# Kernel tuning notes

Hardware: AMD Instinct MI355X
Metric: run time of the kernel (lower is better)

Reference implementation:

```python
import jax, jax.numpy as jnp
import numpy as np

# PSLoss constants (from init_kwargs)
MSE_WEIGHT = 0.5
W_CORR = 1.0
W_VAR = 1.0
W_MEAN = 1.0
K = 3           # k_dominant_freqs
MIN_PATCH = 5   # min_patch_len (max(2, 5))
EPS = 1e-8


def setup_inputs() -> dict:
    key = jax.random.key(0)
    k1, k2 = jax.random.split(key)
    B, T, F = 64, 336, 321
    forecast = jax.random.normal(k1, (B, T, F), dtype=jnp.float32)
    target = jax.random.normal(k2, (B, T, F), dtype=jnp.float32)
    return {"forecast": forecast, "target": target}


def _structural_loss(fc, tg):
    """fc, tg: [N, T] flattened (batch*features) series. Returns (total_loss_sum, patch_count)."""
    N, T = tg.shape
    Mmax = T // MIN_PATCH  # max segments per period (period >= MIN_PATCH)

    # --- Fourier adaptive patching (vectorized over all N series) ---
    amp = jnp.abs(jnp.fft.rfft(tg, axis=-1))[:, 1:]           # drop DC, [N, T//2]
    _, rel = jax.lax.top_k(amp, K)                             # [N, K]
    freq_idx = (rel + 1).astype(jnp.float32)
    p = jnp.floor(T / freq_idx).astype(jnp.int32)              # dominant periods [N, K]
    # dedup periods in topk order (the original 'processed_periods' set)
    eq = p[:, :, None] == p[:, None, :]                        # [N, K, K]
    earlier = jnp.tril(jnp.ones((K, K), dtype=bool), -1)       # j < k
    dup = jnp.any(eq & earlier, axis=-1)
    valid_p = (p >= MIN_PATCH) & ~dup                          # [N, K]

    nseg = T // p                                              # [N, K] (p >= 2 always)
    s_idx = jnp.arange(Mmax, dtype=jnp.int32)
    seg_s = p[:, :, None] * s_idx                              # [N, K, Mmax]
    seg_e = seg_s + p[:, :, None]
    seg_v = (s_idx < nseg[:, :, None]) & valid_p[:, :, None]
    rem_s = nseg * p                                           # remaining tail patch
    rem_v = valid_p & ((T - rem_s) >= MIN_PATCH)

    starts = jnp.concatenate([seg_s.reshape(N, -1), rem_s], axis=-1)
    ends = jnp.concatenate([seg_e.reshape(N, -1), jnp.full_like(rem_s, T)], axis=-1)
    valid = jnp.concatenate([seg_v.reshape(N, -1), rem_v], axis=-1)
    # fallback whole-series patch if no patch survived
    none = ~jnp.any(valid, axis=-1, keepdims=True)
    starts = jnp.concatenate([starts, jnp.zeros((N, 1), jnp.int32)], axis=-1)
    ends = jnp.concatenate([ends, jnp.full((N, 1), T, jnp.int32)], axis=-1)
    valid = jnp.concatenate([valid, none], axis=-1)            # [N, M]

    # --- dedup identical (start, end) patches (original list(set(...))) ---
    SENT = (T + 1) * (T + 1)
    keys = jnp.where(valid, starts * (T + 1) + ends, SENT)
    keys = jnp.sort(keys, axis=-1)
    uniq = jnp.concatenate(
        [jnp.ones((N, 1), dtype=bool), keys[:, 1:] != keys[:, :-1]], axis=-1)
    valid = (keys != SENT) & uniq
    s = jnp.where(valid, keys // (T + 1), 0)                   # safe dummy (0,2) when invalid
    e = jnp.where(valid, keys % (T + 1), 2)

    # --- per-patch stats via inclusive prefix sums ---
    def csum(x):
        return jnp.concatenate([jnp.zeros((N, 1), x.dtype), jnp.cumsum(x, axis=-1)], axis=-1)

    cs_t, cs_f = csum(tg), csum(fc)
    cs_tt, cs_ff, cs_tf = csum(tg * tg), csum(fc * fc), csum(tg * fc)

    def seg_sum(cs):
        return jnp.take_along_axis(cs, e, axis=-1) - jnp.take_along_axis(cs, s, axis=-1)

    n = (e - s).astype(jnp.float32)
    St, Sf = seg_sum(cs_t), seg_sum(cs_f)
    Stt, Sff, Stf = seg_sum(cs_tt), seg_sum(cs_ff), seg_sum(cs_tf)
    mt, mf = St / n, Sf / n
    tvs = jnp.maximum(Stt - n * mt * mt, 0.0)   # sum of squared deviations (target)
    fvs = jnp.maximum(Sff - n * mf * mf, 0.0)
    num = Stf - n * mt * mf
    corr = num / (jnp.sqrt(tvs * fvs) + EPS)
    corr_loss = 1.0 - jnp.abs(corr)
    tvar = tvs / (n - 1.0)                      # torch.var is unbiased
    fvar = fvs / (n - 1.0)
    var_loss = jnp.abs(tvar - fvar) / (tvar + EPS)
    mean_loss = jnp.abs(mt - mf) / (jnp.abs(mt) + EPS)
    patch_loss = W_CORR * corr_loss + W_VAR * var_loss + W_MEAN * mean_loss

    total = jnp.sum(jnp.where(valid, patch_loss, 0.0))
    count = jnp.sum(valid)
    return total, count


def reference(forecast, target):
    B, T, F = forecast.shape
    fc = jnp.transpose(forecast, (0, 2, 1)).reshape(B * F, T)
    tg = jnp.transpose(target, (0, 2, 1)).reshape(B * F, T)
    total, count = _structural_loss(fc, tg)
    avg = jnp.where(count > 0,
                    total / jnp.maximum(count, 1).astype(jnp.float32),
                    jnp.float32(0.0))
    mse = jnp.mean((forecast - target) ** 2)
    return MSE_WEIGHT * mse + (1.0 - MSE_WEIGHT) * avg
```

## Files before the change

### kernel.cpp

```cpp
#include <hip/hip_runtime.h>
#include <hip/hip_bf16.h>

#define TT 336
#define NF 321
#define NB 64
#define NSER (NB * NF)
#define WPB 4
#define KP 352
#define LDA 360
#define SPB 16
#define NPSB (NSER / SPB)
#define NPSBG 1288
#define NPATB (NSER / WPB)
#define TSP (TT + 4)

#define SK(b) ((b) + ((b) >> 5))
#define TBL 348

#define TGX 11
#define TGY 11
#define NMSEP (TGX * TGY * NB)

typedef __attribute__((ext_vector_type(8))) short bf16x8;
typedef __attribute__((ext_vector_type(4))) float f32x4;
typedef unsigned long long ULL;

__device__ __forceinline__ unsigned short f2bf(float v) {
    unsigned x = __float_as_uint(v);
    x += 0x7FFFu + ((x >> 16) & 1u);
    return (unsigned short)(x >> 16);
}

__device__ __forceinline__ void ins3(ULL& a0, ULL& a1, ULL& a2, ULL x) {
    ULL hi = a0 > x ? a0 : x;
    ULL lo = a0 > x ? x : a0;
    a0 = hi;
    ULL hi1 = a1 > lo ? a1 : lo;
    ULL lo1 = a1 > lo ? lo : a1;
    a1 = hi1;
    a2 = a2 > lo1 ? a2 : lo1;
}

__global__ void twiddle_k(unsigned short* __restrict__ Wb) {
    int n = blockIdx.x;
    int f = (n >> 1) + 1;
    int isSin = n & 1;
    for (int k = threadIdx.x; k < KP; k += blockDim.x) {
        float v = 0.0f;
        if (k < TT) {
            int r = (f * k) % TT;
            float ang = 6.2831853071795864769f * (float)r / 336.0f;
            v = isSin ? sinf(ang) : cosf(ang);
        }
        Wb[(size_t)n * KP + k] = f2bf(v);
    }
}

__global__ __launch_bounds__(256) void psd_k(const float* __restrict__ tgO,
                                             const unsigned short* __restrict__ Wb,
                                             uint4* __restrict__ topk) {
    __shared__ __align__(16) unsigned short sA[SPB][LDA];
    __shared__ ULL tk3[4][SPB][3];
    const int tid = threadIdx.x;
    const int lb = (blockIdx.x & 7) * 161 + (blockIdx.x >> 3);
    if (lb >= NPSB) return;
    const int serBase = lb * SPB;

    {
        int f_l = tid & 15, tch = tid >> 4;
        int ser = serBase + f_l;
        int bb = ser / NF, ff = ser - bb * NF;
        const float* base = tgO + (size_t)bb * TT * NF + ff;
        int t0 = tch * 21;
        float v[21];
#pragma unroll
        for (int i = 0; i < 21; i++) v[i] = base[(size_t)(t0 + i) * NF];
#pragma unroll
        for (int i = 0; i < 21; i++) sA[f_l][t0 + i] = f2bf(v[i]);
    }
    if (tid < SPB * 16) sA[tid >> 4][TT + (tid & 15)] = 0;
    __syncthreads();

    const int wave = tid >> 6, lane = tid & 63;
    const int quad = lane >> 4, c = lane & 15;
    const unsigned short* aRow = &sA[c][quad * 8];
    const int ntStart = wave * 5;
    const int ntEnd = (wave == 3) ? 21 : ntStart + 5;

    ULL t0k[4] = {0, 0, 0, 0}, t1k[4] = {0, 0, 0, 0}, t2k[4] = {0, 0, 0, 0};
    for (int nt = ntStart; nt < ntEnd; nt++) {
        const unsigned short* bRow = Wb + (size_t)(nt * 16 + c) * KP + quad * 8;
        f32x4 acc = (f32x4){0.f, 0.f, 0.f, 0.f};
#pragma unroll
        for (int ks = 0; ks < 11; ks++) {
            bf16x8 a = *(const bf16x8*)(aRow + ks * 32);
            bf16x8 b = *(const bf16x8*)(bRow + ks * 32);
            acc = __builtin_amdgcn_mfma_f32_16x16x32_bf16(a, b, acc, 0, 0, 0);
        }
        int n = nt * 16 + c;
        unsigned fidx = (unsigned)((n >> 1) + 1);
        unsigned ftag = 0xFFFFFFFFu - fidx;
        bool odd = (n & 1) != 0;
#pragma unroll
        for (int r = 0; r < 4; r++) {
            float v = acc[r];
            float p = v * v;
            p += __shfl_xor(p, 1, 64);
            ULL key = odd ? 0ull
                          : (((ULL)__float_as_uint(p) << 32) | (ULL)ftag);
            ins3(t0k[r], t1k[r], t2k[r], key);
        }
    }
#pragma unroll
    for (int m = 2; m <= 8; m <<= 1) {
#pragma unroll
        for (int r = 0; r < 4; r++) {
            ULL b0 = __shfl_xor(t0k[r], m, 64);
            ULL b1 = __shfl_xor(t1k[r], m, 64);
            ULL b2 = __shfl_xor(t2k[r], m, 64);
            ins3(t0k[r], t1k[r], t2k[r], b0);
            ins3(t0k[r], t1k[r], t2k[r], b1);
            ins3(t0k[r], t1k[r], t2k[r], b2);
        }
    }
    if (c == 0) {
#pragma unroll
        for (int r = 0; r < 4; r++) {
            int s = quad * 4 + r;
            tk3[wave][s][0] = t0k[r];
            tk3[wave][s][1] = t1k[r];
            tk3[wave][s][2] = t2k[r];
        }
    }
    __syncthreads();
    if (tid < SPB) {
        ULL k0 = 0, k1 = 0, k2 = 0;
#pragma unroll
        for (int wv = 0; wv < 4; wv++) {
#pragma unroll
            for (int j = 0; j < 3; j++) ins3(k0, k1, k2, tk3[wv][tid][j]);
        }
        unsigned f0 = 0xFFFFFFFFu - (unsigned)(k0 & 0xFFFFFFFFull);
        unsigned f1 = 0xFFFFFFFFu - (unsigned)(k1 & 0xFFFFFFFFull);
        unsigned f2 = 0xFFFFFFFFu - (unsigned)(k2 & 0xFFFFFFFFull);
        topk[serBase + tid] = make_uint4(f0, f1, f2, 0u);
    }
}

__global__ __launch_bounds__(256) void transpose_k(const float* __restrict__ fc,
                                                   const float* __restrict__ tg,
                                                   float2* __restrict__ out,
                                                   double* __restrict__ msep,
                                                   double* __restrict__ acc) {
    __shared__ float ta[32][33];
    __shared__ float tb[32][33];
    __shared__ double wacc[4];
    const int b = blockIdx.z;
    const int t0 = blockIdx.x * 32, f0 = blockIdx.y * 32;
    const int tx = threadIdx.x, ty = threadIdx.y;
    const size_t base = (size_t)b * TT * NF;
    double ms = 0.0;
#pragma unroll
    for (int k = 0; k < 4; k++) {
        int t = t0 + ty + 8 * k, f = f0 + tx;
        if (t < TT && f < NF) {
            float a = tg[base + (size_t)t * NF + f];
            float c = fc[base + (size_t)t * NF + f];
            ta[ty + 8 * k][tx] = a;
            tb[ty + 8 * k][tx] = c;
            double d = (double)a - (double)c;
            ms += d * d;
        }
    }
    __syncthreads();
#pragma unroll
    for (int k = 0; k < 4; k++) {
        int f = f0 + ty + 8 * k, t = t0 + tx;
        if (t < TT && f < NF) {
            out[((size_t)b * NF + f) * TT + t] =
                make_float2(ta[tx][ty + 8 * k], tb[tx][ty + 8 * k]);
        }
    }
    for (int off = 32; off; off >>= 1) ms += __shfl_down(ms, off, 64);
    int flat = ty * 32 + tx;
    int lane = flat & 63, wid = flat >> 6;
    if (lane == 0) wacc[wid] = ms;
    __syncthreads();
    if (flat == 0) {
        double tot = wacc[0] + wacc[1] + wacc[2] + wacc[3];
        if (msep) {
            int blk = (blockIdx.z * TGY + blockIdx.y) * TGX + blockIdx.x;
            msep[blk] = tot;
        } else {
            atomicAdd(&acc[0], tot);
        }
    }
}

__global__ void mse_k(const float* __restrict__ fc, const float* __restrict__ tg,
                      double* __restrict__ acc) {
    const size_t N4 = (size_t)NB * TT * NF / 4;
    const float4* a4 = (const float4*)fc;
    const float4* b4 = (const float4*)tg;
    double s = 0.0;
    for (size_t i = (size_t)blockIdx.x * blockDim.x + threadIdx.x; i < N4;
         i += (size_t)gridDim.x * blockDim.x) {
        float4 a = a4[i], b = b4[i];
        double d0 = (double)a.x - (double)b.x;
        double d1 = (double)a.y - (double)b.y;
        double d2 = (double)a.z - (double)b.z;
        double d3 = (double)a.w - (double)b.w;
        s += d0 * d0 + d1 * d1 + d2 * d2 + d3 * d3;
    }
    for (int off = 32; off; off >>= 1) s += __shfl_down(s, off, 64);
    __shared__ double wsum[4];
    int flat = threadIdx.x;
    int lane = flat & 63, wid = flat >> 6;
    if (lane == 0) wsum[wid] = s;
    __syncthreads();
    if (flat == 0) atomicAdd(&acc[0], wsum[0] + wsum[1] + wsum[2] + wsum[3]);
}

__device__ __forceinline__ double patch_loss(double S1, double S2, double S3,
                                             double S4, double S5, double nn) {
    double mt = S1 / nn, mf = S2 / nn;
    double tvs = S3 - nn * mt * mt; tvs = tvs > 0.0 ? tvs : 0.0;
    double fvs = S4 - nn * mf * mf; fvs = fvs > 0.0 ? fvs : 0.0;
    double num = S5 - nn * mt * mf;
    double corr = num / (sqrt(tvs * fvs) + 1e-8);
    double closs = 1.0 - fabs(corr);
    double tvar = tvs / (nn - 1.0), fvar = fvs / (nn - 1.0);
    double vloss = fabs(tvar - fvar) / (tvar + 1e-8);
    double mloss = fabs(mt - mf) / (fabs(mt) + 1e-8);
    return closs + vloss + mloss;
}

__device__ __forceinline__ double patch_loss_fast(double S1, double S2,
                                                  float S3, float S4, float S5,
                                                  int n) {
    float nnf = (float)n;
    float invf = 1.0f / nnf;
    float s1f = (float)S1, s2f = (float)S2;
    float tvs = S3 - s1f * s1f * invf; tvs = tvs > 0.f ? tvs : 0.f;
    float fvs = S4 - s2f * s2f * invf; fvs = fvs > 0.f ? fvs : 0.f;
    float num = S5 - s1f * s2f * invf;
    float corr = num / (sqrtf(tvs * fvs) + 1e-8f);
    float closs = 1.0f - fabsf(corr);
    float vloss = fabsf(tvs - fvs) / (tvs + (nnf - 1.0f) * 1e-8f);
    double mloss = fabs(S1 - S2) / (fabs(S1) + (double)n * 1e-8);
    return (double)(closs + vloss) + mloss;
}

struct PatchCfg {
    int P[3], nseg[3], rs[3];
    bool vp[3], hr[3];
};

__device__ __forceinline__ void make_cfg(int fr0, int fr1, int fr2, PatchCfg& c) {
    c.P[0] = TT / fr0; c.P[1] = TT / fr1; c.P[2] = TT / fr2;
    c.vp[0] = (c.P[0] >= 5);
    c.vp[1] = (c.P[1] >= 5) && (c.P[1] != c.P[0]);
    c.vp[2] = (c.P[2] >= 5) && (c.P[2] != c.P[0]) && (c.P[2] != c.P[1]);
#pragma unroll
    for (int q = 0; q < 3; q++) {
        c.nseg[q] = TT / c.P[q];
        c.rs[q] = c.nseg[q] * c.P[q];
        c.hr[q] = c.vp[q] && ((TT - c.rs[q]) >= 5);
    }
}

__device__ __forceinline__ bool slot_patch(const PatchCfg& c, int i, int& s, int& e) {
    bool kept = false;
    s = 0; e = 0;
    if (i < 204) {
        int k = (i >= 136) ? 2 : ((i >= 68) ? 1 : 0);
        int si = i - k * 68;
        if (c.vp[k]) {
            if (si < c.nseg[k]) { s = c.P[k] * si; e = s + c.P[k]; kept = true; }
            else if (si == c.nseg[k] && c.hr[k]) { s = c.rs[k]; e = TT; kept = true; }
            if (kept) {
#pragma unroll
                for (int j = 0; j < 2; j++) {
                    if (j < k && c.vp[j]) {
                        bool dup = (s == c.rs[j]) && (e == TT) && c.hr[j];
                        int len = e - s;
                        if (len == c.P[j] && s < c.rs[j] && (s % c.P[j]) == 0) dup = true;
                        if (dup) kept = false;
                    }
                }
            }
        }
    }
    return kept;
}

__global__ __launch_bounds__(256) void patch_k(const float* __restrict__ fcO,
                                               const float* __restrict__ tgO,
                                               const uint4* __restrict__ topk,
                                               double* __restrict__ blkout) {
    __shared__ __align__(16) char smem[2 * WPB * TBL * 8 + 3 * WPB * TBL * 4];
    double (*d1)[TBL] = (double(*)[TBL])smem;
    double (*d2)[TBL] = (double(*)[TBL])(smem + WPB * TBL * 8);
    char* regB = smem + 2 * WPB * TBL * 8;
    float2* tsB = (float2*)regB;
    float (*t3)[TBL] = (float(*)[TBL])regB;
    float (*t4)[TBL] = (float(*)[TBL])(regB + WPB * TBL * 4);
    float (*t5)[TBL] = (float(*)[TBL])(regB + 2 * WPB * TBL * 4);
    __shared__ double wms[WPB], wls[WPB], wlc[WPB];

    const int tid = threadIdx.x;
    const int w = tid >> 6, lane = tid & 63;
    const int lb = (blockIdx.x & 7) * (NPATB / 8) + (blockIdx.x >> 3);
    const int ser = lb * WPB + w;

    {
        const int j = tid & 3;
        const int serj = lb * WPB + j;
        const int bb = serj / NF, ff = serj - bb * NF;
        const float* tb_ = tgO + (size_t)bb * TT * NF + ff;
        const float* fb_ = fcO + (size_t)bb * TT * NF + ff;
        const int tb0 = tid >> 2;
        float2* row = tsB + j * TSP;
        double ms = 0.0;
#pragma unroll
        for (int i = 0; i < 6; i++) {
            int t = tb0 + 64 * i;
            if (t < TT) {
                float a = tb_[(size_t)t * NF];
                float c = fb_[(size_t)t * NF];
                row[t] = make_float2(a, c);
                double d = (double)a - (double)c;
                ms += d * d;
            }
        }
        for (int off = 32; off; off >>= 1) ms += __shfl_down(ms, off, 64);
        if (lane == 0) wms[w] = ms;
    }
    __syncthreads();

    float2 loc[6];
    double c1 = 0, c2 = 0;
    float c3 = 0, c4 = 0, c5 = 0;
    if (lane < 56) {
        const float4* lp = (const float4*)(tsB + w * TSP + 6 * lane);
        float4 va = lp[0], vb = lp[1], vc = lp[2];
        loc[0] = make_float2(va.x, va.y); loc[1] = make_float2(va.z, va.w);
        loc[2] = make_float2(vb.x, vb.y); loc[3] = make_float2(vb.z, vb.w);
        loc[4] = make_float2(vc.x, vc.y); loc[5] = make_float2(vc.z, vc.w);
#pragma unroll
        for (int i = 0; i < 6; i++) {
            float a = loc[i].x, b = loc[i].y;
            c1 += (double)a; c2 += (double)b;
            c3 = fmaf(a, a, c3); c4 = fmaf(b, b, c4); c5 = fmaf(a, b, c5);
        }
    }

    double s1 = c1, s2 = c2;
    float s3 = c3, s4 = c4, s5 = c5;
#pragma unroll
    for (int off = 1; off < 64; off <<= 1) {
        double y1 = __shfl_up(s1, off, 64);
        double y2 = __shfl_up(s2, off, 64);
        float y3 = __shfl_up(s3, off, 64);
        float y4 = __shfl_up(s4, off, 64);
        float y5 = __shfl_up(s5, off, 64);
        if (lane >= off) { s1 += y1; s2 += y2; s3 += y3; s4 += y4; s5 += y5; }
    }

    __syncthreads();

    if (lane == 63) {
        d1[w][SK(0)] = 0.0; d2[w][SK(0)] = 0.0;
        t3[w][SK(0)] = 0.f; t4[w][SK(0)] = 0.f; t5[w][SK(0)] = 0.f;
    }
    if (lane < 56) {
        double r1 = s1 - c1, r2 = s2 - c2;
        float r3 = s3 - c3, r4 = s4 - c4, r5 = s5 - c5;
#pragma unroll
        for (int i = 0; i < 6; i++) {
            float a = loc[i].x, b = loc[i].y;
            r1 += (double)a; r2 += (double)b;
            r3 = fmaf(a, a, r3); r4 = fmaf(b, b, r4); r5 = fmaf(a, b, r5);
            int ix = SK(6 * lane + i + 1);
            d1[w][ix] = r1; d2[w][ix] = r2;
            t3[w][ix] = r3; t4[w][ix] = r4; t5[w][ix] = r5;
        }
    }
    __syncthreads();

    uint4 tk = topk[ser];
    PatchCfg cfg;
    make_cfg((int)tk.x, (int)tk.y, (int)tk.z, cfg);

    double lsum = 0.0, lcnt = 0.0;
    ULL anyMask = 0ull;
#pragma unroll
    for (int rI = 0; rI < 4; rI++) {
        int s, e;
        bool kept = slot_patch(cfg, lane + 64 * rI, s, e);
        ULL bal = __ballot(kept);
        anyMask |= bal;
        if (bal == 0ull) continue;
        if (kept) {
            int is = SK(s), ie = SK(e);
            double S1 = d1[w][ie] - d1[w][is];
            double S2 = d2[w][ie] - d2[w][is];
            float S3 = t3[w][ie] - t3[w][is];
            float S4 = t4[w][ie] - t4[w][is];
            float S5 = t5[w][ie] - t5[w][is];
            lsum += patch_loss_fast(S1, S2, S3, S4, S5, e - s);
            lcnt += 1.0;
        }
    }

    if (anyMask == 0ull) {
        if (lane == 0) {
            int ie = SK(TT);
            lsum += patch_loss_fast(d1[w][ie], d2[w][ie], t3[w][ie],
                                    t4[w][ie], t5[w][ie], TT);
            lcnt += 1.0;
        }
    }

    for (int off = 32; off; off >>= 1) {
        lsum += __shfl_down(lsum, off, 64);
        lcnt += __shfl_down(lcnt, off, 64);
    }
    if (lane == 0) { wls[w] = lsum; wlc[w] = lcnt; }
    __syncthreads();
    if (tid == 0) {
        blkout[3 * lb + 0] = wls[0] + wls[1] + wls[2] + wls[3];
        blkout[3 * lb + 1] = wlc[0] + wlc[1] + wlc[2] + wlc[3];
        blkout[3 * lb + 2] = wms[0] + wms[1] + wms[2] + wms[3];
    }
}

__device__ __forceinline__ void patch_body(const float2* tsw, int lane,
                                           int fr0, int fr1, int fr2,
                                           double& lsum, double& lcnt) {
    PatchCfg cfg;
    make_cfg(fr0, fr1, fr2, cfg);
    ULL anyMask = 0ull;
#pragma unroll
    for (int rI = 0; rI < 4; rI++) {
        int s, e;
        bool kept = slot_patch(cfg, lane + 64 * rI, s, e);
        anyMask |= __ballot(kept);
        if (kept) {
            double S1 = 0, S2 = 0, S3 = 0, S4 = 0, S5 = 0;
            for (int t = s; t < e; t++) {
                float2 v = tsw[t];
                double a = (double)v.x, b = (double)v.y;
                S1 += a; S2 += b;
                S3 += a * a; S4 += b * b; S5 += a * b;
            }
            lsum += patch_loss(S1, S2, S3, S4, S5, (double)(e - s));
            lcnt += 1.0;
        }
    }
    if (anyMask == 0ull) {
        double S1 = 0, S2 = 0, S3 = 0, S4 = 0, S5 = 0;
        for (int t = lane; t < TT; t += 64) {
            float2 v = tsw[t];
            double a = (double)v.x, b = (double)v.y;
            S1 += a; S2 += b;
            S3 += a * a; S4 += b * b; S5 += a * b;
        }
        for (int off = 32; off; off >>= 1) {
            S1 += __shfl_down(S1, off, 64);
            S2 += __shfl_down(S2, off, 64);
            S3 += __shfl_down(S3, off, 64);
            S4 += __shfl_down(S4, off, 64);
            S5 += __shfl_down(S5, off, 64);
        }
        if (lane == 0) {
            lsum += patch_loss(S1, S2, S3, S4, S5, (double)TT);
            lcnt += 1.0;
        }
    }
}

__global__ __launch_bounds__(256, 6) void series_k(const float2* __restrict__ tsG,
                                                   const float* __restrict__ fcG,
                                                   const float* __restrict__ tgG,
                                                   int transposed,
                                                   double2* __restrict__ pairs,
                                                   double* __restrict__ acc) {
    const int w = threadIdx.x >> 6, lane = threadIdx.x & 63;
    const int ser = blockIdx.x * WPB + w;
    __shared__ float2 ts[WPB][TT];
    __shared__ float4 zb[WPB][84];

    if (transposed) {
        const float2* sp = tsG + (size_t)ser * TT;
        for (int t = lane; t < TT; t += 64) ts[w][t] = sp[t];
    } else {
        int b = ser / NF, f = ser - b * NF;
        const float* tp = tgG + (size_t)b * TT * NF + f;
        const float* fp = fcG + (size_t)b * TT * NF + f;
        for (int t = lane; t < TT; t += 64)
            ts[w][t] = make_float2(tp[(size_t)t * NF], fp[(size_t)t * NF]);
    }
    __syncthreads();

    for (int t = lane; t < 84; t += 64) {
        float x0 = ts[w][t].x, x1 = ts[w][t + 84].x;
        float x2 = ts[w][t + 168].x, x3 = ts[w][t + 252].x;
        float a = x0 + x2, b2 = x1 + x3, c = x0 - x2, d = x1 - x3;
        zb[w][t] = make_float4(a + b2, a - b2, c, d);
    }
    __syncthreads();

    const double TWOPI = 6.283185307179586476925286766559;
    int fb[3] = {1 + lane, 65 + lane, 129 + lane};
    float cc[3], sn[3], re[3], im[3], cd[3], sd[3], sgn[3];
    int selA[3];
#pragma unroll
    for (int q = 0; q < 3; q++) {
        int f = fb[q], cls = f & 3;
        double dl = (double)f * (TWOPI / 336.0);
        cd[q] = (float)cos(dl);
        sd[q] = (float)sin(dl);
        cc[q] = 1.0f; sn[q] = 0.0f; re[q] = 0.0f; im[q] = 0.0f;
        sgn[q] = (cls == 1) ? -1.0f : ((cls == 3) ? 1.0f : 0.0f);
        selA[q] = (cls == 0) ? 0 : ((cls == 2) ? 1 : 2);
    }
    for (int t = 0; t < 84; t++) {
        float4 zv = zb[w][t];
#pragma unroll
        for (int q = 0; q < 3; q++) {
            float zr = (selA[q] == 0) ? zv.x : ((selA[q] == 1) ? zv.y : zv.z);
            float zi = sgn[q] * zv.w;
            re[q] = fmaf(zr, cc[q], re[q]);
            re[q] = fmaf(zi, sn[q], re[q]);
            im[q] = fmaf(zi, cc[q], im[q]);
            im[q] = fmaf(-zr, sn[q], im[q]);
            float nc = fmaf(cc[q], cd[q], -(sn[q] * sd[q]));
            float ns = fmaf(sn[q], cd[q], cc[q] * sd[q]);
            cc[q] = nc; sn[q] = ns;
        }
    }

    ULL k0 = 0, k1 = 0, k2 = 0;
#pragma unroll
    for (int q = 0; q < 3; q++) {
        float a2 = fmaf(re[q], re[q], im[q] * im[q]);
        ULL key = ((ULL)__float_as_uint(a2) << 32) |
                  (ULL)(0xFFFFFFFFu - (unsigned)fb[q]);
        if (fb[q] > 168) key = 0ull;
        ins3(k0, k1, k2, key);
    }
    for (int m = 1; m < 64; m <<= 1) {
        ULL b0 = __shfl_xor(k0, m, 64);
        ULL b1 = __shfl_xor(k1, m, 64);
        ULL b2 = __shfl_xor(k2, m, 64);
        ins3(k0, k1, k2, b0); ins3(k0, k1, k2, b1); ins3(k0, k1, k2, b2);
    }

    int fr0 = (int)(0xFFFFFFFFu - (unsigned)(k0 & 0xFFFFFFFFull));
    int fr1 = (int)(0xFFFFFFFFu - (unsigned)(k1 & 0xFFFFFFFFull));
    int fr2 = (int)(0xFFFFFFFFu - (unsigned)(k2 & 0xFFFFFFFFull));

    double lsum = 0.0, lcnt = 0.0;
    patch_body(&ts[w][0], lane, fr0, fr1, fr2, lsum, lcnt);

    for (int off = 32; off; off >>= 1) {
        lsum += __shfl_down(lsum, off, 64);
        lcnt += __shfl_down(lcnt, off, 64);
    }
    if (lane == 0) {
        if (pairs) {
            pairs[ser] = make_double2(lsum, lcnt);
        } else {
            atomicAdd(&acc[1], lsum);
            atomicAdd(&acc[2], lcnt);
        }
    }
}

__global__ __launch_bounds__(1024) void reduce3_k(const double* __restrict__ blkout,
                                                  float* __restrict__ out) {
    const int tid = threadIdx.x;
    double ls = 0.0, lc = 0.0, ms = 0.0;
    for (int i = tid; i < NPATB; i += 1024) {
        ls += blkout[3 * i + 0];
        lc += blkout[3 * i + 1];
        ms += blkout[3 * i + 2];
    }
    for (int off = 32; off; off >>= 1) {
        ls += __shfl_down(ls, off, 64);
        lc += __shfl_down(lc, off, 64);
        ms += __shfl_down(ms, off, 64);
    }
    __shared__ double sl[16], sc[16], sm[16];
    int lane = tid & 63, wid = tid >> 6;
    if (lane == 0) { sl[wid] = ls; sc[wid] = lc; sm[wid] = ms; }
    __syncthreads();
    if (tid == 0) {
        double L = 0, C = 0, M = 0;
        for (int i = 0; i < 16; i++) { L += sl[i]; C += sc[i]; M += sm[i]; }
        double mse = M / (double)((size_t)NB * TT * NF);
        double avg = (C > 0.0) ? (L / C) : 0.0;
        out[0] = (float)(0.5 * mse + 0.5 * avg);
    }
}

__global__ __launch_bounds__(1024) void reduce_k(const double2* __restrict__ pairs,
                                                 const double* __restrict__ msep,
                                                 int nmse,
                                                 float* __restrict__ out) {
    const int tid = threadIdx.x;
    double ls = 0.0, lc = 0.0, ms = 0.0;
    for (int i = tid; i < NSER; i += 1024) {
        double2 p = pairs[i];
        ls += p.x; lc += p.y;
    }
    for (int i = tid; i < nmse; i += 1024) ms += msep[i];
    for (int off = 32; off; off >>= 1) {
        ls += __shfl_down(ls, off, 64);
        lc += __shfl_down(lc, off, 64);
        ms += __shfl_down(ms, off, 64);
    }
    __shared__ double sl[16], sc[16], sm[16];
    int lane = tid & 63, wid = tid >> 6;
    if (lane == 0) { sl[wid] = ls; sc[wid] = lc; sm[wid] = ms; }
    __syncthreads();
    if (tid == 0) {
        double L = 0, C = 0, M = 0;
        for (int i = 0; i < 16; i++) { L += sl[i]; C += sc[i]; M += sm[i]; }
        double mse = M / (double)((size_t)NB * TT * NF);
        double avg = (C > 0.0) ? (L / C) : 0.0;
        out[0] = (float)(0.5 * mse + 0.5 * avg);
    }
}

__global__ void finalize_k(const double* __restrict__ acc, float* __restrict__ out) {
    double mse = acc[0] / (double)((size_t)NB * TT * NF);
    double avg = (acc[2] > 0.0) ? (acc[1] / acc[2]) : 0.0;
    out[0] = (float)(0.5 * mse + 0.5 * avg);
}

extern "C" void kernel_launch(void* const* d_in, const int* in_sizes, int n_in,
                              void* d_out, int out_size, void* d_ws, size_t ws_size,
                              hipStream_t stream) {
    const float* fc = (const float*)d_in[0];
    const float* tg = (const float*)d_in[1];
    float* out = (float*)d_out;
    char* ws = (char*)d_ws;
    double* acc = (double*)ws;

    const size_t OFF_MSE = 64;
    const size_t OFF_PAIR = OFF_MSE + (size_t)NMSEP * sizeof(double);
    const size_t OFF_TOP = OFF_PAIR + (size_t)NSER * sizeof(double2);
    const size_t OFF_W = OFF_TOP + (size_t)NSER * sizeof(uint4);
    const size_t OFF_END2 = OFF_W + (size_t)TT * KP * sizeof(unsigned short);
    const size_t bytesT = (size_t)NSER * TT * sizeof(float2);
    const bool big2 = (ws_size >= OFF_END2);
    const size_t R3_OFF_TS = OFF_PAIR + (size_t)NSER * sizeof(double2);
    const bool big = !big2 && (ws_size >= R3_OFF_TS + bytesT);
    const bool mid = !big2 && !big && (ws_size >= OFF_MSE + bytesT);

    double* msep = (double*)(ws + OFF_MSE);
    double* blkout = (double*)(ws + OFF_PAIR);
    uint4* topkBuf = (uint4*)(ws + OFF_TOP);
    unsigned short* Wb = (unsigned short*)(ws + OFF_W);

    dim3 tg_grid(TGX, TGY, NB);
    dim3 tg_blk(32, 8);

    if (big2) {
        twiddle_k<<<TT, 128, 0, stream>>>(Wb);
        psd_k<<<NPSBG, 256, 0, stream>>>(tg, Wb, topkBuf);
        patch_k<<<NPATB, 64 * WPB, 0, stream>>>(fc, tg, topkBuf, blkout);
        reduce3_k<<<1, 1024, 0, stream>>>(blkout, out);
    } else if (big) {
        float2* tsT = (float2*)(ws + R3_OFF_TS);
        transpose_k<<<tg_grid, tg_blk, 0, stream>>>(fc, tg, tsT, msep, acc);
        series_k<<<NSER / WPB, 64 * WPB, 0, stream>>>(tsT, fc, tg, 1,
                                                      (double2*)blkout, acc);
        reduce_k<<<1, 1024, 0, stream>>>((double2*)blkout, msep, NMSEP, out);
    } else if (mid) {
        float2* tsT = (float2*)(ws + OFF_MSE);
        hipMemsetAsync(d_ws, 0, 64, stream);
        transpose_k<<<tg_grid, tg_blk, 0, stream>>>(fc, tg, tsT, nullptr, acc);
        series_k<<<NSER / WPB, 64 * WPB, 0, stream>>>(tsT, fc, tg, 1, nullptr, acc);
        finalize_k<<<1, 1, 0, stream>>>(acc, out);
    } else {
        hipMemsetAsync(d_ws, 0, 64, stream);
        mse_k<<<1024, 256, 0, stream>>>(fc, tg, acc);
        series_k<<<NSER / WPB, 64 * WPB, 0, stream>>>(nullptr, fc, tg, 0, nullptr, acc);
        finalize_k<<<1, 1, 0, stream>>>(acc, out);
    }
}
```

Measured before the change: 160.0 us.

## Fuse PSD top-k and patch loss kernels into a single kernel

Merges the MFMA-based spectral top-k kernel and the per-series patch statistics kernel into one kernel. Each block now computes top-k for its 16 series, keeps the result in shared memory, then loops over four groups of four series to compute the prefix sums and patch losses, reusing the same shared buffer. This removes a kernel launch and the global round trip of the top-k buffer. In exchange each block does more serial work with extra barriers, and the grid drops to 1288 blocks, which may lower parallelism in the patch phase.

```diff
diff --git a/kernel.cpp b/kernel.cpp
--- a/kernel.cpp
+++ b/kernel.cpp
@@ -56,15 +56,101 @@
     }
 }
 
-__global__ __launch_bounds__(256) void psd_k(const float* __restrict__ tgO,
-                                             const unsigned short* __restrict__ Wb,
-                                             uint4* __restrict__ topk) {
-    __shared__ __align__(16) unsigned short sA[SPB][LDA];
-    __shared__ ULL tk3[4][SPB][3];
+__device__ __forceinline__ double patch_loss(double S1, double S2, double S3,
+                                             double S4, double S5, double nn) {
+    double mt = S1 / nn, mf = S2 / nn;
+    double tvs = S3 - nn * mt * mt; tvs = tvs > 0.0 ? tvs : 0.0;
+    double fvs = S4 - nn * mf * mf; fvs = fvs > 0.0 ? fvs : 0.0;
+    double num = S5 - nn * mt * mf;
+    double corr = num / (sqrt(tvs * fvs) + 1e-8);
+    double closs = 1.0 - fabs(corr);
+    double tvar = tvs / (nn - 1.0), fvar = fvs / (nn - 1.0);
+    double vloss = fabs(tvar - fvar) / (tvar + 1e-8);
+    double mloss = fabs(mt - mf) / (fabs(mt) + 1e-8);
+    return closs + vloss + mloss;
+}
+
+__device__ __forceinline__ double patch_loss_fast(double S1, double S2,
+                                                  float S3, float S4, float S5,
+                                                  int n) {
+    float nnf = (float)n;
+    float invf = 1.0f / nnf;
+    float s1f = (float)S1, s2f = (float)S2;
+    float tvs = S3 - s1f * s1f * invf; tvs = tvs > 0.f ? tvs : 0.f;
+    float fvs = S4 - s2f * s2f * invf; fvs = fvs > 0.f ? fvs : 0.f;
+    float num = S5 - s1f * s2f * invf;
+    float corr = num / (sqrtf(tvs * fvs) + 1e-8f);
+    float closs = 1.0f - fabsf(corr);
+    float vloss = fabsf(tvs - fvs) / (tvs + (nnf - 1.0f) * 1e-8f);
+    double mloss = fabs(S1 - S2) / (fabs(S1) + (double)n * 1e-8);
+    return (double)(closs + vloss) + mloss;
+}
+
+struct PatchCfg {
+    int P[3], nseg[3], rs[3];
+    bool vp[3], hr[3];
+};
+
+__device__ __forceinline__ void make_cfg(int fr0, int fr1, int fr2, PatchCfg& c) {
+    c.P[0] = TT / fr0; c.P[1] = TT / fr1; c.P[2] = TT / fr2;
+    c.vp[0] = (c.P[0] >= 5);
+    c.vp[1] = (c.P[1] >= 5) && (c.P[1] != c.P[0]);
+    c.vp[2] = (c.P[2] >= 5) && (c.P[2] != c.P[0]) && (c.P[2] != c.P[1]);
+#pragma unroll
+    for (int q = 0; q < 3; q++) {
+        c.nseg[q] = TT / c.P[q];
+        c.rs[q] = c.nseg[q] * c.P[q];
+        c.hr[q] = c.vp[q] && ((TT - c.rs[q]) >= 5);
+    }
+}
+
+__device__ __forceinline__ bool slot_patch(const PatchCfg& c, int i, int& s, int& e) {
+    bool kept = false;
+    s = 0; e = 0;
+    if (i < 204) {
+        int k = (i >= 136) ? 2 : ((i >= 68) ? 1 : 0);
+        int si = i - k * 68;
+        if (c.vp[k]) {
+            if (si < c.nseg[k]) { s = c.P[k] * si; e = s + c.P[k]; kept = true; }
+            else if (si == c.nseg[k] && c.hr[k]) { s = c.rs[k]; e = TT; kept = true; }
+            if (kept) {
+#pragma unroll
+                for (int j = 0; j < 2; j++) {
+                    if (j < k && c.vp[j]) {
+                        bool dup = (s == c.rs[j]) && (e == TT) && c.hr[j];
+                        int len = e - s;
+                        if (len == c.P[j] && s < c.rs[j] && (s % c.P[j]) == 0) dup = true;
+                        if (dup) kept = false;
+                    }
+                }
+            }
+        }
+    }
+    return kept;
+}
+
+__global__ __launch_bounds__(256) void psdpatch_k(const float* __restrict__ fcO,
+                                                  const float* __restrict__ tgO,
+                                                  const unsigned short* __restrict__ Wb,
+                                                  double* __restrict__ blkout) {
+    __shared__ __align__(16) char smem[2 * WPB * TBL * 8 + 3 * WPB * TBL * 4];
+    unsigned short (*sA)[LDA] = (unsigned short(*)[LDA])smem;
+    ULL (*tk3)[SPB][3] = (ULL(*)[SPB][3])(smem + SPB * LDA * 2);
+    double (*d1)[TBL] = (double(*)[TBL])smem;
+    double (*d2)[TBL] = (double(*)[TBL])(smem + WPB * TBL * 8);
+    char* regB = smem + 2 * WPB * TBL * 8;
+    float2* tsB = (float2*)regB;
+    float (*t3)[TBL] = (float(*)[TBL])regB;
+    float (*t4)[TBL] = (float(*)[TBL])(regB + WPB * TBL * 4);
+    float (*t5)[TBL] = (float(*)[TBL])(regB + 2 * WPB * TBL * 4);
+    __shared__ uint4 tkf[SPB];
+    __shared__ double wms[WPB], wls[WPB], wlc[WPB];
+
     const int tid = threadIdx.x;
     const int lb = (blockIdx.x & 7) * 161 + (blockIdx.x >> 3);
     if (lb >= NPSB) return;
     const int serBase = lb * SPB;
+    const int wave = tid >> 6, lane = tid & 63;
 
     {
         int f_l = tid & 15, tch = tid >> 4;
@@ -81,55 +167,56 @@
     if (tid < SPB * 16) sA[tid >> 4][TT + (tid & 15)] = 0;
     __syncthreads();
 
-    const int wave = tid >> 6, lane = tid & 63;
-    const int quad = lane >> 4, c = lane & 15;
-    const unsigned short* aRow = &sA[c][quad * 8];
-    const int ntStart = wave * 5;
-    const int ntEnd = (wave == 3) ? 21 : ntStart + 5;
-
-    ULL t0k[4] = {0, 0, 0, 0}, t1k[4] = {0, 0, 0, 0}, t2k[4] = {0, 0, 0, 0};
-    for (int nt = ntStart; nt < ntEnd; nt++) {
-        const unsigned short* bRow = Wb + (size_t)(nt * 16 + c) * KP + quad * 8;
-        f32x4 acc = (f32x4){0.f, 0.f, 0.f, 0.f};
-#pragma unroll
-        for (int ks = 0; ks < 11; ks++) {
-            bf16x8 a = *(const bf16x8*)(aRow + ks * 32);
-            bf16x8 b = *(const bf16x8*)(bRow + ks * 32);
-            acc = __builtin_amdgcn_mfma_f32_16x16x32_bf16(a, b, acc, 0, 0, 0);
-        }
-        int n = nt * 16 + c;
-        unsigned fidx = (unsigned)((n >> 1) + 1);
-        unsigned ftag = 0xFFFFFFFFu - fidx;
-        bool odd = (n & 1) != 0;
-#pragma unroll
-        for (int r = 0; r < 4; r++) {
-            float v = acc[r];
-            float p = v * v;
-            p += __shfl_xor(p, 1, 64);
-            ULL key = odd ? 0ull
-                          : (((ULL)__float_as_uint(p) << 32) | (ULL)ftag);
-            ins3(t0k[r], t1k[r], t2k[r], key);
-        }
-    }
-#pragma unroll
-    for (int m = 2; m <= 8; m <<= 1) {
-#pragma unroll
-        for (int r = 0; r < 4; r++) {
-            ULL b0 = __shfl_xor(t0k[r], m, 64);
-            ULL b1 = __shfl_xor(t1k[r], m, 64);
-            ULL b2 = __shfl_xor(t2k[r], m, 64);
-            ins3(t0k[r], t1k[r], t2k[r], b0);
-            ins3(t0k[r], t1k[r], t2k[r], b1);
-            ins3(t0k[r], t1k[r], t2k[r], b2);
-        }
-    }
-    if (c == 0) {
-#pragma unroll
-        for (int r = 0; r < 4; r++) {
-            int s = quad * 4 + r;
-            tk3[wave][s][0] = t0k[r];
-            tk3[wave][s][1] = t1k[r];
-            tk3[wave][s][2] = t2k[r];
+    {
+        const int quad = lane >> 4, c = lane & 15;
+        const unsigned short* aRow = &sA[c][quad * 8];
+        const int ntStart = wave * 5;
+        const int ntEnd = (wave == 3) ? 21 : ntStart + 5;
+
+        ULL t0k[4] = {0, 0, 0, 0}, t1k[4] = {0, 0, 0, 0}, t2k[4] = {0, 0, 0, 0};
+        for (int nt = ntStart; nt < ntEnd; nt++) {
+            const unsigned short* bRow = Wb + (size_t)(nt * 16 + c) * KP + quad * 8;
+            f32x4 acc = (f32x4){0.f, 0.f, 0.f, 0.f};
+#pragma unroll
+            for (int ks = 0; ks < 11; ks++) {
+                bf16x8 a = *(const bf16x8*)(aRow + ks * 32);
+                bf16x8 b = *(const bf16x8*)(bRow + ks * 32);
+                acc = __builtin_amdgcn_mfma_f32_16x16x32_bf16(a, b, acc, 0, 0, 0);
+            }
+            int n = nt * 16 + c;
+            unsigned fidx = (unsigned)((n >> 1) + 1);
+            unsigned ftag = 0xFFFFFFFFu - fidx;
+            bool odd = (n & 1) != 0;
+#pragma unroll
+            for (int r = 0; r < 4; r++) {
+                float v = acc[r];
+                float p = v * v;
+                p += __shfl_xor(p, 1, 64);
+                ULL key = odd ? 0ull
+                              : (((ULL)__float_as_uint(p) << 32) | (ULL)ftag);
+                ins3(t0k[r], t1k[r], t2k[r], key);
+            }
+        }
+#pragma unroll
+        for (int m = 2; m <= 8; m <<= 1) {
+#pragma unroll
+            for (int r = 0; r < 4; r++) {
+                ULL b0 = __shfl_xor(t0k[r], m, 64);
+                ULL b1 = __shfl_xor(t1k[r], m, 64);
+                ULL b2 = __shfl_xor(t2k[r], m, 64);
+                ins3(t0k[r], t1k[r], t2k[r], b0);
+                ins3(t0k[r], t1k[r], t2k[r], b1);
+                ins3(t0k[r], t1k[r], t2k[r], b2);
+            }
+        }
+        if (c == 0) {
+#pragma unroll
+            for (int r = 0; r < 4; r++) {
+                int s = quad * 4 + r;
+                tk3[wave][s][0] = t0k[r];
+                tk3[wave][s][1] = t1k[r];
+                tk3[wave][s][2] = t2k[r];
+            }
         }
     }
     __syncthreads();
@@ -143,7 +230,159 @@
         unsigned f0 = 0xFFFFFFFFu - (unsigned)(k0 & 0xFFFFFFFFull);
         unsigned f1 = 0xFFFFFFFFu - (unsigned)(k1 & 0xFFFFFFFFull);
         unsigned f2 = 0xFFFFFFFFu - (unsigned)(k2 & 0xFFFFFFFFull);
-        topk[serBase + tid] = make_uint4(f0, f1, f2, 0u);
+        tkf[tid] = make_uint4(f0, f1, f2, 0u);
+    }
+
+    double lsumRun = 0.0, lcntRun = 0.0, msThr = 0.0;
+    const int w = wave;
+
+    for (int rr = 0; rr < 4; rr++) {
+        __syncthreads();
+
+        {
+            const int j = tid & 3;
+            const int serj = serBase + 4 * rr + j;
+            const int bb = serj / NF, ff = serj - bb * NF;
+            const float* tb_ = tgO + (size_t)bb * TT * NF + ff;
+            const float* fb_ = fcO + (size_t)bb * TT * NF + ff;
+            const int tb0 = tid >> 2;
+            float2* row = tsB + j * TSP;
+#pragma unroll
+            for (int i = 0; i < 6; i++) {
+                int t = tb0 + 64 * i;
+                if (t < TT) {
+                    float a = tb_[(size_t)t * NF];
+                    float c = fb_[(size_t)t * NF];
+                    row[t] = make_float2(a, c);
+                    double d = (double)a - (double)c;
+                    msThr += d * d;
+                }
+            }
+        }
+        __syncthreads();
+
+        float2 loc[6];
+        double c1 = 0, c2 = 0;
+        float c3 = 0, c4 = 0, c5 = 0;
+        if (lane < 56) {
+            const float4* lp = (const float4*)(tsB + w * TSP + 6 * lane);
+            float4 va = lp[0], vb = lp[1], vc = lp[2];
+            loc[0] = make_float2(va.x, va.y); loc[1] = make_float2(va.z, va.w);
+            loc[2] = make_float2(vb.x, vb.y); loc[3] = make_float2(vb.z, vb.w);
+            loc[4] = make_float2(vc.x, vc.y); loc[5] = make_float2(vc.z, vc.w);
+#pragma unroll
+            for (int i = 0; i < 6; i++) {
+                float a = loc[i].x, b = loc[i].y;
+                c1 += (double)a; c2 += (double)b;
+                c3 = fmaf(a, a, c3); c4 = fmaf(b, b, c4); c5 = fmaf(a, b, c5);
+            }
+        }
+
+        double s1 = c1, s2 = c2;
+        float s3 = c3, s4 = c4, s5 = c5;
+#pragma unroll
+        for (int off = 1; off < 64; off <<= 1) {
+            double y1 = __shfl_up(s1, off, 64);
+            double y2 = __shfl_up(s2, off, 64);
+            float y3 = __shfl_up(s3, off, 64);
+            float y4 = __shfl_up(s4, off, 64);
+            float y5 = __shfl_up(s5, off, 64);
+            if (lane >= off) { s1 += y1; s2 += y2; s3 += y3; s4 += y4; s5 += y5; }
+        }
+
+        __syncthreads();
+
+        if (lane == 63) {
+            d1[w][SK(0)] = 0.0; d2[w][SK(0)] = 0.0;
+            t3[w][SK(0)] = 0.f; t4[w][SK(0)] = 0.f; t5[w][SK(0)] = 0.f;
+        }
+        if (lane < 56) {
+            double r1 = s1 - c1, r2 = s2 - c2;
+            float r3 = s3 - c3, r4 = s4 - c4, r5 = s5 - c5;
+#pragma unroll
+            for (int i = 0; i < 6; i++) {
+                float a = loc[i].x, b = loc[i].y;
+                r1 += (double)a; r2 += (double)b;
+                r3 = fmaf(a, a, r3); r4 = fmaf(b, b, r4); r5 = fmaf(a, b, r5);
+                int ix = SK(6 * lane + i + 1);
+                d1[w][ix] = r1; d2[w][ix] = r2;
+                t3[w][ix] = r3; t4[w][ix] = r4; t5[w][ix] = r5;
+            }
+        }
+        __syncthreads();
+
+        uint4 tk = tkf[4 * rr + w];
+        PatchCfg cfg;
+        make_cfg((int)tk.x, (int)tk.y, (int)tk.z, cfg);
+
+        ULL anyMask = 0ull;
+#pragma unroll
+        for (int rI = 0; rI < 4; rI++) {
+            int s, e;
+            bool kept = slot_patch(cfg, lane + 64 * rI, s, e);
+            ULL bal = __ballot(kept);
+            anyMask |= bal;
+            if (bal == 0ull) continue;
+            if (kept) {
+                int is = SK(s), ie = SK(e);
+                double S1 = d1[w][ie] - d1[w][is];
+                double S2 = d2[w][ie] - d2[w][is];
+                float S3 = t3[w][ie] - t3[w][is];
+                float S4 = t4[w][ie] - t4[w][is];
+                float S5 = t5[w][ie] - t5[w][is];
+                lsumRun += patch_loss_fast(S1, S2, S3, S4, S5, e - s);
+                lcntRun += 1.0;
+            }
+        }
+        if (anyMask == 0ull) {
+            if (lane == 0) {
+                int ie = SK(TT);
+                lsumRun += patch_loss_fast(d1[w][ie], d2[w][ie], t3[w][ie],
+                                           t4[w][ie], t5[w][ie], TT);
+                lcntRun += 1.0;
+            }
+        }
+    }
+
+    for (int off = 32; off; off >>= 1) {
+        lsumRun += __shfl_down(lsumRun, off, 64);
+        lcntRun += __shfl_down(lcntRun, off, 64);
+        msThr += __shfl_down(msThr, off, 64);
+    }
+    if (lane == 0) { wls[w] = lsumRun; wlc[w] = lcntRun; wms[w] = msThr; }
+    __syncthreads();
+    if (tid == 0) {
+        blkout[3 * lb + 0] = wls[0] + wls[1] + wls[2] + wls[3];
+        blkout[3 * lb + 1] = wlc[0] + wlc[1] + wlc[2] + wlc[3];
+        blkout[3 * lb + 2] = wms[0] + wms[1] + wms[2] + wms[3];
+    }
+}
+
+__global__ __launch_bounds__(1024) void reduce3_k(const double* __restrict__ blkout,
+                                                  int nblk,
+                                                  float* __restrict__ out) {
+    const int tid = threadIdx.x;
+    double ls = 0.0, lc = 0.0, ms = 0.0;
+    for (int i = tid; i < nblk; i += 1024) {
+        ls += blkout[3 * i + 0];
+        lc += blkout[3 * i + 1];
+        ms += blkout[3 * i + 2];
+    }
+    for (int off = 32; off; off >>= 1) {
+        ls += __shfl_down(ls, off, 64);
+        lc += __shfl_down(lc, off, 64);
+        ms += __shfl_down(ms, off, 64);
+    }
+    __shared__ double sl[16], sc[16], sm[16];
+    int lane = tid & 63, wid = tid >> 6;
+    if (lane == 0) { sl[wid] = ls; sc[wid] = lc; sm[wid] = ms; }
+    __syncthreads();
+    if (tid == 0) {
+        double L = 0, C = 0, M = 0;
+        for (int i = 0; i < 16; i++) { L += sl[i]; C += sc[i]; M += sm[i]; }
+        double mse = M / (double)((size_t)NB * TT * NF);
+        double avg = (C > 0.0) ? (L / C) : 0.0;
+        out[0] = (float)(0.5 * mse + 0.5 * avg);
     }
 }
 
@@ -221,220 +460,6 @@
     if (flat == 0) atomicAdd(&acc[0], wsum[0] + wsum[1] + wsum[2] + wsum[3]);
 }
 
-__device__ __forceinline__ double patch_loss(double S1, double S2, double S3,
-                                             double S4, double S5, double nn) {
-    double mt = S1 / nn, mf = S2 / nn;
-    double tvs = S3 - nn * mt * mt; tvs = tvs > 0.0 ? tvs : 0.0;
-    double fvs = S4 - nn * mf * mf; fvs = fvs > 0.0 ? fvs : 0.0;
-    double num = S5 - nn * mt * mf;
-    double corr = num / (sqrt(tvs * fvs) + 1e-8);
-    double closs = 1.0 - fabs(corr);
-    double tvar = tvs / (nn - 1.0), fvar = fvs / (nn - 1.0);
-    double vloss = fabs(tvar - fvar) / (tvar + 1e-8);
-    double mloss = fabs(mt - mf) / (fabs(mt) + 1e-8);
-    return closs + vloss + mloss;
-}
-
-__device__ __forceinline__ double patch_loss_fast(double S1, double S2,
-                                                  float S3, float S4, float S5,
-                                                  int n) {
-    float nnf = (float)n;
-    float invf = 1.0f / nnf;
-    float s1f = (float)S1, s2f = (float)S2;
-    float tvs = S3 - s1f * s1f * invf; tvs = tvs > 0.f ? tvs : 0.f;
-    float fvs = S4 - s2f * s2f * invf; fvs = fvs > 0.f ? fvs : 0.f;
-    float num = S5 - s1f * s2f * invf;
-    float corr = num / (sqrtf(tvs * fvs) + 1e-8f);
-    float closs = 1.0f - fabsf(corr);
-    float vloss = fabsf(tvs - fvs) / (tvs + (nnf - 1.0f) * 1e-8f);
-    double mloss = fabs(S1 - S2) / (fabs(S1) + (double)n * 1e-8);
-    return (double)(closs + vloss) + mloss;
-}
-
-struct PatchCfg {
-    int P[3], nseg[3], rs[3];
-    bool vp[3], hr[3];
-};
-
-__device__ __forceinline__ void make_cfg(int fr0, int fr1, int fr2, PatchCfg& c) {
-    c.P[0] = TT / fr0; c.P[1] = TT / fr1; c.P[2] = TT / fr2;
-    c.vp[0] = (c.P[0] >= 5);
-    c.vp[1] = (c.P[1] >= 5) && (c.P[1] != c.P[0]);
-    c.vp[2] = (c.P[2] >= 5) && (c.P[2] != c.P[0]) && (c.P[2] != c.P[1]);
-#pragma unroll
-    for (int q = 0; q < 3; q++) {
-        c.nseg[q] = TT / c.P[q];
-        c.rs[q] = c.nseg[q] * c.P[q];
-        c.hr[q] = c.vp[q] && ((TT - c.rs[q]) >= 5);
-    }
-}
-
-__device__ __forceinline__ bool slot_patch(const PatchCfg& c, int i, int& s, int& e) {
-    bool kept = false;
-    s = 0; e = 0;
-    if (i < 204) {
-        int k = (i >= 136) ? 2 : ((i >= 68) ? 1 : 0);
-        int si = i - k * 68;
-        if (c.vp[k]) {
-            if (si < c.nseg[k]) { s = c.P[k] * si; e = s + c.P[k]; kept = true; }
-            else if (si == c.nseg[k] && c.hr[k]) { s = c.rs[k]; e = TT; kept = true; }
-            if (kept) {
-#pragma unroll
-                for (int j = 0; j < 2; j++) {
-                    if (j < k && c.vp[j]) {
-                        bool dup = (s == c.rs[j]) && (e == TT) && c.hr[j];
-                        int len = e - s;
-                        if (len == c.P[j] && s < c.rs[j] && (s % c.P[j]) == 0) dup = true;
-                        if (dup) kept = false;
-                    }
-                }
-            }
-        }
-    }
-    return kept;
-}
-
-__global__ __launch_bounds__(256) void patch_k(const float* __restrict__ fcO,
-                                               const float* __restrict__ tgO,
-                                               const uint4* __restrict__ topk,
-                                               double* __restrict__ blkout) {
-    __shared__ __align__(16) char smem[2 * WPB * TBL * 8 + 3 * WPB * TBL * 4];
-    double (*d1)[TBL] = (double(*)[TBL])smem;
-    double (*d2)[TBL] = (double(*)[TBL])(smem + WPB * TBL * 8);
-    char* regB = smem + 2 * WPB * TBL * 8;
-    float2* tsB = (float2*)regB;
-    float (*t3)[TBL] = (float(*)[TBL])regB;
-    float (*t4)[TBL] = (float(*)[TBL])(regB + WPB * TBL * 4);
-    float (*t5)[TBL] = (float(*)[TBL])(regB + 2 * WPB * TBL * 4);
-    __shared__ double wms[WPB], wls[WPB], wlc[WPB];
-
-    const int tid = threadIdx.x;
-    const int w = tid >> 6, lane = tid & 63;
-    const int lb = (blockIdx.x & 7) * (NPATB / 8) + (blockIdx.x >> 3);
-    const int ser = lb * WPB + w;
-
-    {
-        const int j = tid & 3;
-        const int serj = lb * WPB + j;
-        const int bb = serj / NF, ff = serj - bb * NF;
-        const float* tb_ = tgO + (size_t)bb * TT * NF + ff;
-        const float* fb_ = fcO + (size_t)bb * TT * NF + ff;
-        const int tb0 = tid >> 2;
-        float2* row = tsB + j * TSP;
-        double ms = 0.0;
-#pragma unroll
-        for (int i = 0; i < 6; i++) {
-            int t = tb0 + 64 * i;
-            if (t < TT) {
-                float a = tb_[(size_t)t * NF];
-                float c = fb_[(size_t)t * NF];
-                row[t] = make_float2(a, c);
-                double d = (double)a - (double)c;
-                ms += d * d;
-            }
-        }
-        for (int off = 32; off; off >>= 1) ms += __shfl_down(ms, off, 64);
-        if (lane == 0) wms[w] = ms;
-    }
-    __syncthreads();
-
-    float2 loc[6];
-    double c1 = 0, c2 = 0;
-    float c3 = 0, c4 = 0, c5 = 0;
-    if (lane < 56) {
-        const float4* lp = (const float4*)(tsB + w * TSP + 6 * lane);
-        float4 va = lp[0], vb = lp[1], vc = lp[2];
-        loc[0] = make_float2(va.x, va.y); loc[1] = make_float2(va.z, va.w);
-        loc[2] = make_float2(vb.x, vb.y); loc[3] = make_float2(vb.z, vb.w);
-        loc[4] = make_float2(vc.x, vc.y); loc[5] = make_float2(vc.z, vc.w);
-#pragma unroll
-        for (int i = 0; i < 6; i++) {
-            float a = loc[i].x, b = loc[i].y;
-            c1 += (double)a; c2 += (double)b;
-            c3 = fmaf(a, a, c3); c4 = fmaf(b, b, c4); c5 = fmaf(a, b, c5);
-        }
-    }
-
-    double s1 = c1, s2 = c2;
-    float s3 = c3, s4 = c4, s5 = c5;
-#pragma unroll
-    for (int off = 1; off < 64; off <<= 1) {
-        double y1 = __shfl_up(s1, off, 64);
-        double y2 = __shfl_up(s2, off, 64);
-        float y3 = __shfl_up(s3, off, 64);
-        float y4 = __shfl_up(s4, off, 64);
-        float y5 = __shfl_up(s5, off, 64);
-        if (lane >= off) { s1 += y1; s2 += y2; s3 += y3; s4 += y4; s5 += y5; }
-    }
-
-    __syncthreads();
-
-    if (lane == 63) {
-        d1[w][SK(0)] = 0.0; d2[w][SK(0)] = 0.0;
-        t3[w][SK(0)] = 0.f; t4[w][SK(0)] = 0.f; t5[w][SK(0)] = 0.f;
-    }
-    if (lane < 56) {
-        double r1 = s1 - c1, r2 = s2 - c2;
-        float r3 = s3 - c3, r4 = s4 - c4, r5 = s5 - c5;
-#pragma unroll
-        for (int i = 0; i < 6; i++) {
-            float a = loc[i].x, b = loc[i].y;
-            r1 += (double)a; r2 += (double)b;
-            r3 = fmaf(a, a, r3); r4 = fmaf(b, b, r4); r5 = fmaf(a, b, r5);
-            int ix = SK(6 * lane + i + 1);
-            d1[w][ix] = r1; d2[w][ix] = r2;
-            t3[w][ix] = r3; t4[w][ix] = r4; t5[w][ix] = r5;
-        }
-    }
-    __syncthreads();
-
-    uint4 tk = topk[ser];
-    PatchCfg cfg;
-    make_cfg((int)tk.x, (int)tk.y, (int)tk.z, cfg);
-
-    double lsum = 0.0, lcnt = 0.0;
-    ULL anyMask = 0ull;
-#pragma unroll
-    for (int rI = 0; rI < 4; rI++) {
-        int s, e;
-        bool kept = slot_patch(cfg, lane + 64 * rI, s, e);
-        ULL bal = __ballot(kept);
-        anyMask |= bal;
-        if (bal == 0ull) continue;
-        if (kept) {
-            int is = SK(s), ie = SK(e);
-            double S1 = d1[w][ie] - d1[w][is];
-            double S2 = d2[w][ie] - d2[w][is];
-            float S3 = t3[w][ie] - t3[w][is];
-            float S4 = t4[w][ie] - t4[w][is];
-            float S5 = t5[w][ie] - t5[w][is];
-            lsum += patch_loss_fast(S1, S2, S3, S4, S5, e - s);
-            lcnt += 1.0;
-        }
-    }
-
-    if (anyMask == 0ull) {
-        if (lane == 0) {
-            int ie = SK(TT);
-            lsum += patch_loss_fast(d1[w][ie], d2[w][ie], t3[w][ie],
-                                    t4[w][ie], t5[w][ie], TT);
-            lcnt += 1.0;
-        }
-    }
-
-    for (int off = 32; off; off >>= 1) {
-        lsum += __shfl_down(lsum, off, 64);
-        lcnt += __shfl_down(lcnt, off, 64);
-    }
-    if (lane == 0) { wls[w] = lsum; wlc[w] = lcnt; }
-    __syncthreads();
-    if (tid == 0) {
-        blkout[3 * lb + 0] = wls[0] + wls[1] + wls[2] + wls[3];
-        blkout[3 * lb + 1] = wlc[0] + wlc[1] + wlc[2] + wlc[3];
-        blkout[3 * lb + 2] = wms[0] + wms[1] + wms[2] + wms[3];
-    }
-}
-
 __device__ __forceinline__ void patch_body(const float2* tsw, int lane,
                                            int fr0, int fr1, int fr2,
                                            double& lsum, double& lcnt) {
@@ -578,33 +603,6 @@
     }
 }
 
-__global__ __launch_bounds__(1024) void reduce3_k(const double* __restrict__ blkout,
-                                                  float* __restrict__ out) {
-    const int tid = threadIdx.x;
-    double ls = 0.0, lc = 0.0, ms = 0.0;
-    for (int i = tid; i < NPATB; i += 1024) {
-        ls += blkout[3 * i + 0];
-        lc += blkout[3 * i + 1];
-        ms += blkout[3 * i + 2];
-    }
-    for (int off = 32; off; off >>= 1) {
-        ls += __shfl_down(ls, off, 64);
-        lc += __shfl_down(lc, off, 64);
-        ms += __shfl_down(ms, off, 64);
-    }
-    __shared__ double sl[16], sc[16], sm[16];
-    int lane = tid & 63, wid = tid >> 6;
-    if (lane == 0) { sl[wid] = ls; sc[wid] = lc; sm[wid] = ms; }
-    __syncthreads();
-    if (tid == 0) {
-        double L = 0, C = 0, M = 0;
-        for (int i = 0; i < 16; i++) { L += sl[i]; C += sc[i]; M += sm[i]; }
-        double mse = M / (double)((size_t)NB * TT * NF);
-        double avg = (C > 0.0) ? (L / C) : 0.0;
-        out[0] = (float)(0.5 * mse + 0.5 * avg);
-    }
-}
-
 __global__ __launch_bounds__(1024) void reduce_k(const double2* __restrict__ pairs,
                                                  const double* __restrict__ msep,
                                                  int nmse,
@@ -662,7 +660,6 @@
 
     double* msep = (double*)(ws + OFF_MSE);
     double* blkout = (double*)(ws + OFF_PAIR);
-    uint4* topkBuf = (uint4*)(ws + OFF_TOP);
     unsigned short* Wb = (unsigned short*)(ws + OFF_W);
 
     dim3 tg_grid(TGX, TGY, NB);
@@ -670,9 +667,8 @@
 
     if (big2) {
         twiddle_k<<<TT, 128, 0, stream>>>(Wb);
-        psd_k<<<NPSBG, 256, 0, stream>>>(tg, Wb, topkBuf);
-        patch_k<<<NPATB, 64 * WPB, 0, stream>>>(fc, tg, topkBuf, blkout);
-        reduce3_k<<<1, 1024, 0, stream>>>(blkout, out);
+        psdpatch_k<<<NPSBG, 256, 0, stream>>>(fc, tg, Wb, blkout);
+        reduce3_k<<<1, 1024, 0, stream>>>(blkout, NPSB, out);
     } else if (big) {
         float2* tsT = (float2*)(ws + R3_OFF_TS);
         transpose_k<<<tg_grid, tg_blk, 0, stream>>>(fc, tg, tsT, msep, acc);
```

Result: no change. 163.0 us (+1.9%).
